# Kernel tuning notes

Hardware: AMD Instinct MI355X
Metric: run time of the kernel (lower is better)

The kernel has to match this reference:

```python
import jax, jax.numpy as jnp
import numpy as np

C = 16      # internal_channel
DG = 8      # deform groups
KK = 9      # 3x3 kernel


def conv2d(x, w, b, pad):
    out = jax.lax.conv_general_dilated(
        x, w, (1, 1), [(pad, pad), (pad, pad)],
        dimension_numbers=('NCHW', 'OIHW', 'NCHW'))
    return out + b[None, :, None, None]


def feature_extraction(img, w1, b1, w2, b2, w3, b3):
    f1 = jax.nn.relu(conv2d(img, w1, b1, 1))   # [B,C,H,W]
    f2 = jax.nn.relu(conv2d(f1, w2, b2, 0))    # [B,C,H-2,W-2]
    f3 = jax.nn.relu(conv2d(f2, w3, b3, 0))    # [B,C,H-4,W-4]
    return [f1, f2, f3]


def deform_conv(x, offset, w, b):
    # x: [B,C,H,W]; offset: [B, DG*KK*2, H, W] (y,x pairs); w: [Cout,C,3,3]
    B, Cin, H, W = x.shape
    Cg = Cin // DG
    off = offset.reshape(B, DG, KK, 2, H, W)
    ky = jnp.repeat(jnp.arange(3) - 1, 3)  # kernel y offsets (pad=1)
    kx = jnp.tile(jnp.arange(3) - 1, 3)
    base_y = jnp.arange(H).reshape(1, 1, 1, H, 1)
    base_x = jnp.arange(W).reshape(1, 1, 1, 1, W)
    sy = base_y + ky.reshape(1, 1, KK, 1, 1) + off[:, :, :, 0]  # [B,DG,KK,H,W]
    sx = base_x + kx.reshape(1, 1, KK, 1, 1) + off[:, :, :, 1]
    y0 = jnp.floor(sy)
    x0 = jnp.floor(sx)
    wy = (sy - y0)[:, :, None]  # [B,DG,1,KK,H,W]
    wx = (sx - x0)[:, :, None]
    y0i = y0.astype(jnp.int32)
    x0i = x0.astype(jnp.int32)
    xg = x.reshape(B, DG, Cg, H * W)

    def gather(yy, xx):
        valid = (yy >= 0) & (yy < H) & (xx >= 0) & (xx < W)  # zero pad outside
        idx = (jnp.clip(yy, 0, H - 1) * W + jnp.clip(xx, 0, W - 1))
        idx_b = jnp.broadcast_to(idx.reshape(B, DG, 1, KK, H * W), (B, DG, Cg, KK, H * W))
        src = jnp.broadcast_to(xg[:, :, :, None, :], (B, DG, Cg, KK, H * W))
        g = jnp.take_along_axis(src, idx_b, axis=-1).reshape(B, DG, Cg, KK, H, W)
        return g * valid[:, :, None].astype(x.dtype)

    v00 = gather(y0i, x0i)
    v01 = gather(y0i, x0i + 1)
    v10 = gather(y0i + 1, x0i)
    v11 = gather(y0i + 1, x0i + 1)
    s = (v00 * (1 - wy) * (1 - wx) + v01 * (1 - wy) * wx
         + v10 * wy * (1 - wx) + v11 * wy * wx)
    s = s.reshape(B, Cin, KK, H, W)
    out = jnp.einsum('bckhw,ock->bohw', s, w.reshape(w.shape[0], Cin, KK))
    return out + b[None, :, None, None]


def setup_inputs() -> dict:
    key = jax.random.key(0)
    ks = jax.random.split(key, 24)
    B, H, W = 4, 192, 192
    sc = 0.05
    d = {
        'ref_image': jax.random.normal(ks[0], (B, C, H, W), jnp.float32),
        'unreg_image': jax.random.normal(ks[1], (B, C, H, W), jnp.float32),
        'fe_w1': jax.random.normal(ks[2], (C, C, 3, 3), jnp.float32) * sc,
        'fe_b1': jnp.zeros((C,), jnp.float32),
        'fe_w2': jax.random.normal(ks[3], (C, C, 3, 3), jnp.float32) * sc,
        'fe_b2': jnp.zeros((C,), jnp.float32),
        'fe_w3': jax.random.normal(ks[4], (C, C, 3, 3), jnp.float32) * sc,
        'fe_b3': jnp.zeros((C,), jnp.float32),
        'off_w0': jax.random.normal(ks[5], (C, 2 * C, 3, 3), jnp.float32) * sc,
        'off_b0': jnp.zeros((C,), jnp.float32),
        'off_w1': jax.random.normal(ks[6], (C, 2 * C, 3, 3), jnp.float32) * sc,
        'off_b1': jnp.zeros((C,), jnp.float32),
        'off_w2': jax.random.normal(ks[7], (C, 2 * C, 3, 3), jnp.float32) * sc,
        'off_b2': jnp.zeros((C,), jnp.float32),
        'dcn_off_w': jax.random.normal(ks[8], (2 * DG * KK, C, 3, 3), jnp.float32) * sc,
        'dcn_off_b': jnp.zeros((2 * DG * KK,), jnp.float32),
        'dcn_w': jax.random.normal(ks[9], (C, C, 3, 3), jnp.float32) * sc,
        'dcn_b': jnp.zeros((C,), jnp.float32),
    }
    return d


def reference(ref_image, unreg_image, fe_w1, fe_b1, fe_w2, fe_b2, fe_w3, fe_b3,
              off_w0, off_b0, off_w1, off_b1, off_w2, off_b2,
              dcn_off_w, dcn_off_b, dcn_w, dcn_b):
    ref_f = feature_extraction(ref_image, fe_w1, fe_b1, fe_w2, fe_b2, fe_w3, fe_b3)
    unr_f = feature_extraction(unreg_image, fe_w1, fe_b1, fe_w2, fe_b2, fe_w3, fe_b3)
    off_ws = [(off_w0, off_b0), (off_w1, off_b1), (off_w2, off_b2)]
    aligned = [None, None, None]
    for i in range(2, -1, -1):  # coarse-to-fine as in the source loop
        cat = jnp.concatenate([ref_f[i], unr_f[i]], axis=1)        # [B,2C,h,w]
        off_feat = jax.nn.relu(conv2d(cat, off_ws[i][0], off_ws[i][1], 1))
        offsets = conv2d(off_feat, dcn_off_w, dcn_off_b, 1)        # [B,2*DG*KK,h,w]
        aligned[i] = deform_conv(unr_f[i], offsets, dcn_w, dcn_b)
    return tuple(aligned)
```

## Files before the change

### kernel.cpp

```cpp
#include <hip/hip_runtime.h>

typedef unsigned int uint;
typedef unsigned short ushort;
typedef __attribute__((ext_vector_type(8))) short bf16x8;
typedef __attribute__((ext_vector_type(4))) float f32x4;

__device__ inline ushort f2bf(float f) {
    uint u = __float_as_uint(f);
    u += 0x7fff + ((u >> 16) & 1);
    return (ushort)(u >> 16);
}
__device__ inline float bflo(uint w) { return __uint_as_float(w << 16); }
__device__ inline float bfhi(uint w) { return __uint_as_float(w & 0xffff0000u); }

__global__ void packall_k(
    const float* __restrict__ fe_w1, const float* __restrict__ fe_w2,
    const float* __restrict__ fe_w3, const float* __restrict__ off_w0,
    const float* __restrict__ off_w1, const float* __restrict__ off_w2,
    const float* __restrict__ dcn_off_w, const float* __restrict__ dcn_w,
    ushort* __restrict__ pf1, ushort* __restrict__ pf2, ushort* __restrict__ pf3,
    ushort* __restrict__ po0, ushort* __restrict__ po1, ushort* __restrict__ po2,
    ushort* __restrict__ pow_, ushort* __restrict__ pd) {
    const int y = blockIdx.y;
    int i = blockIdx.x * 256 + threadIdx.x;
    const float* w; ushort* pk; int CIN, NT, KS;
    switch (y) {
        case 0: w = fe_w1;  pk = pf1;  CIN = 16; NT = 1; KS = 5; break;
        case 1: w = fe_w2;  pk = pf2;  CIN = 16; NT = 1; KS = 5; break;
        case 2: w = fe_w3;  pk = pf3;  CIN = 16; NT = 1; KS = 5; break;
        case 3: w = off_w0; pk = po0;  CIN = 32; NT = 1; KS = 9; break;
        case 4: w = off_w1; pk = po1;  CIN = 32; NT = 1; KS = 9; break;
        case 5: w = off_w2; pk = po2;  CIN = 32; NT = 1; KS = 9; break;
        case 6: w = dcn_off_w; pk = pow_; CIN = 16; NT = 9; KS = 5; break;
        default: w = dcn_w; pk = pd;   CIN = 16; NT = 1; KS = 5; break;
    }
    if (i >= KS * NT * 512) return;
    int e = i & 7, lane = (i >> 3) & 63, rest = i >> 9;
    int nt = rest % NT, ks = rest / NT;
    int k = ks * 32 + (lane >> 4) * 8 + e;
    int n = nt * 16 + (lane & 15);
    int t, ci;
    if (CIN == 16) { t = k >> 4; ci = k & 15; } else { t = k >> 5; ci = k & 31; }
    float v = (t < 9) ? w[(n * CIN + ci) * 9 + t] : 0.f;
    pk[i] = f2bf(v);
}

template <bool PLANAR>
__launch_bounds__(256)
__global__ void fe_mfma_k(const float* __restrict__ pA, const float* __restrict__ pB,
                          const ushort* __restrict__ catin,
                          const ushort* __restrict__ pack, const float* __restrict__ bias,
                          ushort* __restrict__ catout,
                          int H, int W, int OH, int OW, int pad) {
    __shared__ ushort patch[324 * 16];
    const int tid = threadIdx.x;
    const int tx0 = blockIdx.x * 16, ty0 = blockIdx.y * 16;
    const int b = blockIdx.z & 3, img = blockIdx.z >> 2;
    const int bx = tx0 - pad, by = ty0 - pad;
    const int HW = H * W;

    if (PLANAR) {
        const float* inb = (img ? pB : pA) + (size_t)(b * 16) * HW;
        for (int pos = tid; pos < 324; pos += 256) {
            int r = pos / 18, c = pos - r * 18;
            int gy = by + r, gx = bx + c;
            bool ok = (unsigned)gy < (unsigned)H && (unsigned)gx < (unsigned)W;
            int base = gy * W + gx;
            uint o16[8];
#pragma unroll
            for (int ii = 0; ii < 8; ++ii) {
                float lo = ok ? inb[(2 * ii) * HW + base] : 0.f;
                float hi = ok ? inb[(2 * ii + 1) * HW + base] : 0.f;
                o16[ii] = (uint)f2bf(lo) | ((uint)f2bf(hi) << 16);
            }
            *(uint4*)(patch + pos * 16) = *(uint4*)&o16[0];
            *(uint4*)(patch + pos * 16 + 8) = *(uint4*)&o16[4];
        }
    } else {
        for (int c = tid; c < 648; c += 256) {
            int pos = c >> 1, h = c & 1;
            int r = pos / 18, col = pos - r * 18;
            int gy = by + r, gx = bx + col;
            uint4 v = make_uint4(0, 0, 0, 0);
            if ((unsigned)gy < (unsigned)H && (unsigned)gx < (unsigned)W)
                v = *(const uint4*)(catin + ((size_t)(b * H + gy) * W + gx) * 32 + img * 16 + h * 8);
            *(uint4*)(patch + pos * 16 + h * 8) = v;
        }
    }
    __syncthreads();

    const int lane = tid & 63, wv = tid >> 6;
    const int g = lane >> 4, ci0 = (g & 1) * 8, rowx = lane & 15;
    f32x4 acc[4];
    float bv = bias[rowx];
#pragma unroll
    for (int m = 0; m < 4; ++m) acc[m] = f32x4{bv, bv, bv, bv};

#pragma unroll
    for (int ks = 0; ks < 5; ++ks) {
        int t = 2 * ks + (g >> 1);
        int dy = t < 9 ? t / 3 : 0;
        int dx = t < 9 ? t - (t / 3) * 3 : 0;
        bf16x8 a[4];
#pragma unroll
        for (int m = 0; m < 4; ++m) {
            int r = wv * 4 + m + dy, cc = rowx + dx;
            a[m] = *(const bf16x8*)(patch + (r * 18 + cc) * 16 + ci0);
        }
        bf16x8 bfrag = *(const bf16x8*)((const uint4*)pack + ks * 64 + lane);
#pragma unroll
        for (int m = 0; m < 4; ++m)
            acc[m] = __builtin_amdgcn_mfma_f32_16x16x32_bf16(a[m], bfrag, acc[m], 0, 0, 0);
    }

    const int oxb = g * 4;
#pragma unroll
    for (int m = 0; m < 4; ++m) {
        int gy = ty0 + wv * 4 + m;
        if (gy >= OH) continue;
#pragma unroll
        for (int j = 0; j < 4; ++j) {
            int gx = tx0 + oxb + j;
            if (gx < OW)
                catout[((size_t)(b * OH + gy) * OW + gx) * 32 + img * 16 + rowx] =
                    f2bf(fmaxf(acc[m][j], 0.f));
        }
    }
}

__launch_bounds__(256)
__global__ void off_mfma_k(const ushort* __restrict__ c0, const ushort* __restrict__ c1,
                           const ushort* __restrict__ c2,
                           const ushort* __restrict__ pk0, const ushort* __restrict__ pk1,
                           const ushort* __restrict__ pk2,
                           const float* __restrict__ b0, const float* __restrict__ b1,
                           const float* __restrict__ b2,
                           ushort* __restrict__ f0, ushort* __restrict__ f1,
                           ushort* __restrict__ f2) {
    const int z = blockIdx.z, s = z >> 2, b = z & 3;
    const int H = 192 - 2 * s, W = H;
    const ushort* cat  = s == 0 ? c0 : (s == 1 ? c1 : c2);
    const ushort* pack = s == 0 ? pk0 : (s == 1 ? pk1 : pk2);
    const float* bias  = s == 0 ? b0 : (s == 1 ? b1 : b2);
    ushort* out        = s == 0 ? f0 : (s == 1 ? f1 : f2);

    __shared__ ushort patch[324 * 32];
    const int tid = threadIdx.x;
    const int tx0 = blockIdx.x * 16, ty0 = blockIdx.y * 16;
    const int bx = tx0 - 1, by = ty0 - 1;

    for (int c = tid; c < 1296; c += 256) {
        int pos = c >> 2, h = c & 3;
        int r = pos / 18, col = pos - r * 18;
        int gy = by + r, gx = bx + col;
        uint4 v = make_uint4(0, 0, 0, 0);
        if ((unsigned)gy < (unsigned)H && (unsigned)gx < (unsigned)W)
            v = *(const uint4*)(cat + ((size_t)(b * H + gy) * W + gx) * 32 + h * 8);
        *(uint4*)(patch + pos * 32 + h * 8) = v;
    }
    __syncthreads();

    const int lane = tid & 63, wv = tid >> 6;
    const int g = lane >> 4, ci0 = g * 8, rowx = lane & 15;
    f32x4 acc[4];
    float bv = bias[rowx];
#pragma unroll
    for (int m = 0; m < 4; ++m) acc[m] = f32x4{bv, bv, bv, bv};

#pragma unroll
    for (int ks = 0; ks < 9; ++ks) {
        int dy = ks / 3, dx = ks - (ks / 3) * 3;
        bf16x8 a[4];
#pragma unroll
        for (int m = 0; m < 4; ++m) {
            int r = wv * 4 + m + dy, cc = rowx + dx;
            a[m] = *(const bf16x8*)(patch + (r * 18 + cc) * 32 + ci0);
        }
        bf16x8 bfrag = *(const bf16x8*)((const uint4*)pack + ks * 64 + lane);
#pragma unroll
        for (int m = 0; m < 4; ++m)
            acc[m] = __builtin_amdgcn_mfma_f32_16x16x32_bf16(a[m], bfrag, acc[m], 0, 0, 0);
    }

    const int oxb = g * 4;
#pragma unroll
    for (int m = 0; m < 4; ++m) {
        int gy = ty0 + wv * 4 + m;
        if (gy >= H) continue;
#pragma unroll
        for (int j = 0; j < 4; ++j) {
            int gx = tx0 + oxb + j;
            if (gx < W)
                out[((size_t)(b * H + gy) * W + gx) * 16 + rowx] = f2bf(fmaxf(acc[m][j], 0.f));
        }
    }
}

__launch_bounds__(256)
__global__ void offconv_mfma_k(const ushort* __restrict__ fb0, const ushort* __restrict__ fb1,
                               const ushort* __restrict__ fb2,
                               const ushort* __restrict__ owPack, const float* __restrict__ ob,
                               ushort* __restrict__ of0, ushort* __restrict__ of1,
                               ushort* __restrict__ of2, int zbase) {
    const int z = blockIdx.z + zbase;
    const int s = z >> 2, b = z & 3;
    const int H = 192 - 2 * s, W = H;
    const ushort* fb = s == 0 ? fb0 : (s == 1 ? fb1 : fb2);
    ushort* ofs = s == 0 ? of0 : (s == 1 ? of1 : of2);

    __shared__ ushort smem[10240];
    ushort* patch = smem;
    const int tid = threadIdx.x;
    const int tx0 = blockIdx.x * 16, ty0 = blockIdx.y * 16;

    for (int c = tid; c < 648; c += 256) {
        int pos = c >> 1, h = c & 1;
        int r = pos / 18, col = pos - r * 18;
        int gy = ty0 - 1 + r, gx = tx0 - 1 + col;
        uint4 v = make_uint4(0, 0, 0, 0);
        if (gy >= 0 && gy < H && gx >= 0 && gx < W)
            v = *(const uint4*)(fb + ((size_t)(b * H + gy) * W + gx) * 16 + h * 8);
        *(uint4*)(patch + pos * 16 + h * 8) = v;
    }
    __syncthreads();

    const int lane = tid & 63, wv = tid >> 6;
    const int g = lane >> 4, ci0 = (g & 1) * 8, rowx = lane & 15;

    f32x4 acc[4][9];
#pragma unroll
    for (int n = 0; n < 9; ++n) {
        float bv = ob[n * 16 + rowx];
#pragma unroll
        for (int m = 0; m < 4; ++m) acc[m][n] = f32x4{bv, bv, bv, bv};
    }

#pragma unroll
    for (int ks = 0; ks < 5; ++ks) {
        int t = 2 * ks + (g >> 1);
        int dy = t < 9 ? t / 3 : 0;
        int dx = t < 9 ? t - (t / 3) * 3 : 0;
        bf16x8 a[4];
#pragma unroll
        for (int m = 0; m < 4; ++m) {
            int r = wv * 4 + m + dy, cc = rowx + dx;
            a[m] = *(const bf16x8*)(patch + (r * 18 + cc) * 16 + ci0);
        }
        const uint4* bp = (const uint4*)owPack + (size_t)(ks * 9) * 64 + lane;
#pragma unroll
        for (int n = 0; n < 9; ++n) {
            bf16x8 bfrag = *(const bf16x8*)(bp + (size_t)n * 64);
#pragma unroll
            for (int m = 0; m < 4; ++m)
                acc[m][n] = __builtin_amdgcn_mfma_f32_16x16x32_bf16(a[m], bfrag, acc[m][n], 0, 0, 0);
        }
    }
    __syncthreads();

    ushort* ot = smem + wv * 2560;
    const size_t rowbytes_base = (size_t)b * H * W;
#pragma unroll
    for (int m = 0; m < 4; ++m) {
#pragma unroll
        for (int n = 0; n < 9; ++n) {
            int ch = n * 16 + rowx;
            int dg = ch / 18;
            int rem = ch - dg * 18;
            int col = (rem >> 1) * 16 + dg * 2 + (rem & 1);
#pragma unroll
            for (int j = 0; j < 4; ++j)
                ot[(g * 4 + j) * 160 + col] = f2bf(acc[m][n][j]);
        }
        int py = ty0 + wv * 4 + m;
        if (py < H) {
            const uint4* src4 = (const uint4*)ot;
            uint4* dst4 = (uint4*)(ofs + (rowbytes_base + (size_t)py * W + tx0) * 160);
            for (int i = lane; i < 320; i += 64)
                if (tx0 + i / 20 < W) dst4[i] = src4[i];
        }
    }
}

__launch_bounds__(256)
__global__ void sample_mfma_k(const ushort* __restrict__ c0, const ushort* __restrict__ c1,
                              const ushort* __restrict__ c2,
                              const ushort* __restrict__ of0, const ushort* __restrict__ of1,
                              const ushort* __restrict__ of2,
                              const ushort* __restrict__ pd, const float* __restrict__ db,
                              float* __restrict__ o0, float* __restrict__ o1,
                              float* __restrict__ o2, int zbase) {
    const int z = blockIdx.z + zbase;
    const int s = z >> 2, b = z & 3;
    const int H = 192 - 2 * s, W = H;
    const ushort* cat = s == 0 ? c0 : (s == 1 ? c1 : c2);
    const ushort* ofs = s == 0 ? of0 : (s == 1 ? of1 : of2);
    float* out = s == 0 ? o0 : (s == 1 ? o1 : o2);
    const int HW = H * W;
    const size_t pixb = (size_t)b * HW;

    __shared__ float2 xt[8][22 * 22];
    const int tid = threadIdx.x;
    const int tx0 = blockIdx.x * 16, ty0 = blockIdx.y * 16;
    const int bx = tx0 - 3, by = ty0 - 3;

    for (int pos = tid; pos < 484; pos += 256) {
        int r = pos / 22, c = pos - r * 22;
        int gy2 = by + r, gx2 = bx + c;
        uint4 va = make_uint4(0, 0, 0, 0), vb = va;
        if ((unsigned)gy2 < (unsigned)H && (unsigned)gx2 < (unsigned)W) {
            const ushort* src = cat + (pixb + gy2 * W + gx2) * 32 + 16;
            va = *(const uint4*)src;
            vb = *(const uint4*)(src + 8);
        }
        uint u[8] = {va.x, va.y, va.z, va.w, vb.x, vb.y, vb.z, vb.w};
#pragma unroll
        for (int cp = 0; cp < 8; ++cp)
            xt[cp][pos] = make_float2(bflo(u[cp]), bfhi(u[cp]));
    }
    __syncthreads();

    const int lane = tid & 63, wv = tid >> 6;
    const int g = lane >> 4, rowx = lane & 15, half = g & 1;
    const int px = tx0 + rowx;
    const int pxc = px < W ? px : W - 1;

    f32x4 acc[4];
    float bv = db[rowx];
#pragma unroll
    for (int m = 0; m < 4; ++m) acc[m] = f32x4{bv, bv, bv, bv};

#pragma unroll 1
    for (int ks = 0; ks < 5; ++ks) {
        const int t = 2 * ks + (g >> 1);
        const bool tv = (t < 9);
        const int t3 = t / 3;
        const int ky = (tv ? t3 : 0) - 1, kx = (tv ? t - t3 * 3 : 0) - 1;

        uint4 ovm[4];
#pragma unroll
        for (int m = 0; m < 4; ++m) {
            int py = ty0 + wv * 4 + m;
            int pyc = py < H ? py : H - 1;
            ovm[m] = tv ? *(const uint4*)(ofs + (pixb + pyc * W + pxc) * 160 + t * 16 + half * 8)
                        : make_uint4(0, 0, 0, 0);
        }
        bf16x8 bfrag = *(const bf16x8*)((const uint4*)pd + ks * 64 + lane);

#pragma unroll
        for (int m = 0; m < 4; ++m) {
            const int py = ty0 + wv * 4 + m;
            uint ovv[4] = {ovm[m].x, ovm[m].y, ovm[m].z, ovm[m].w};
            uint a2[4];
            if (tv) {
#pragma unroll
                for (int d = 0; d < 4; ++d) {
                    const int dgA = half * 4 + d;
                    uint u = ovv[d];
                    float sy = (float)(py + ky) + bflo(u);
                    float sx = (float)(px + kx) + bfhi(u);
                    float fy = floorf(sy), fx = floorf(sx);
                    int y0 = (int)fy, x0 = (int)fx;
                    float wy = sy - fy, wx = sx - fx;
                    float wy1 = 1.f - wy, wx1 = 1.f - wx;
                    float w00 = wy1 * wx1, w01 = wy1 * wx, w10 = wy * wx1, w11 = wy * wx;
                    int ly = y0 - by, lx = x0 - bx;
                    float2 v00, v01, v10, v11;
                    if ((unsigned)ly <= 20u && (unsigned)lx <= 20u) {
                        const float2* tt = &xt[dgA][ly * 22 + lx];
                        v00 = tt[0]; v01 = tt[1]; v10 = tt[22]; v11 = tt[23];
                    } else {
                        v00 = v01 = v10 = v11 = make_float2(0.f, 0.f);
                        bool y0v = (unsigned)y0 < (unsigned)H;
                        bool y1v = (unsigned)(y0 + 1) < (unsigned)H;
                        bool x0v = (unsigned)x0 < (unsigned)W;
                        bool x1v = (unsigned)(x0 + 1) < (unsigned)W;
                        const ushort* cg = cat + ((size_t)pixb + (size_t)y0 * W + x0) * 32 + 16 + 2 * dgA;
                        if (y0v && x0v) { uint uu = *(const uint*)cg;                 v00 = make_float2(bflo(uu), bfhi(uu)); }
                        if (y0v && x1v) { uint uu = *(const uint*)(cg + 32);          v01 = make_float2(bflo(uu), bfhi(uu)); }
                        if (y1v && x0v) { uint uu = *(const uint*)(cg + 32 * W);      v10 = make_float2(bflo(uu), bfhi(uu)); }
                        if (y1v && x1v) { uint uu = *(const uint*)(cg + 32 * W + 32); v11 = make_float2(bflo(uu), bfhi(uu)); }
                    }
                    float s0 = w00 * v00.x + w01 * v01.x + w10 * v10.x + w11 * v11.x;
                    float s1 = w00 * v00.y + w01 * v01.y + w10 * v10.y + w11 * v11.y;
                    a2[d] = (uint)f2bf(s0) | ((uint)f2bf(s1) << 16);
                }
            } else {
                a2[0] = a2[1] = a2[2] = a2[3] = 0u;
            }
            uint4 av = make_uint4(a2[0], a2[1], a2[2], a2[3]);
            bf16x8 af = *(bf16x8*)&av;
            acc[m] = __builtin_amdgcn_mfma_f32_16x16x32_bf16(af, bfrag, acc[m], 0, 0, 0);
        }
    }

#pragma unroll
    for (int m = 0; m < 4; ++m) {
        int py = ty0 + wv * 4 + m;
        if (py >= H) continue;
        float* op = out + (size_t)(b * 16 + rowx) * HW + (size_t)py * W;
#pragma unroll
        for (int j = 0; j < 4; ++j) {
            int gx2 = tx0 + g * 4 + j;
            if (gx2 < W) op[gx2] = acc[m][j];
        }
    }
}

extern "C" void kernel_launch(void* const* d_in, const int* in_sizes, int n_in,
                              void* d_out, int out_size, void* d_ws, size_t ws_size,
                              hipStream_t stream) {
    const float* ref_image = (const float*)d_in[0];
    const float* unreg_image = (const float*)d_in[1];
    const float* fe_w1 = (const float*)d_in[2];
    const float* fe_b1 = (const float*)d_in[3];
    const float* fe_w2 = (const float*)d_in[4];
    const float* fe_b2 = (const float*)d_in[5];
    const float* fe_w3 = (const float*)d_in[6];
    const float* fe_b3 = (const float*)d_in[7];
    const float* off_w0 = (const float*)d_in[8];
    const float* off_b0 = (const float*)d_in[9];
    const float* off_w1 = (const float*)d_in[10];
    const float* off_b1 = (const float*)d_in[11];
    const float* off_w2 = (const float*)d_in[12];
    const float* off_b2 = (const float*)d_in[13];
    const float* dcn_off_w = (const float*)d_in[14];
    const float* dcn_off_b = (const float*)d_in[15];
    const float* dcn_w = (const float*)d_in[16];
    const float* dcn_b = (const float*)d_in[17];

    const size_t pix[3] = {4ul * 192 * 192, 4ul * 190 * 190, 4ul * 188 * 188};
    const size_t szf[3] = {pix[0] * 16, pix[1] * 16, pix[2] * 16};

    size_t o = 0;
    auto take = [&](size_t bytes) {
        void* r = (char*)d_ws + o;
        o += (bytes + 255) & ~(size_t)255;
        return r;
    };
    ushort* cat[3]; ushort* fb[3];
    ushort* pf[3]; ushort* po[3]; ushort* owPack; ushort* pd;
    for (int s = 0; s < 3; ++s) cat[s] = (ushort*)take(pix[s] * 32 * 2);
    for (int s = 0; s < 3; ++s) fb[s] = (ushort*)take(pix[s] * 16 * 2);
    for (int s = 0; s < 3; ++s) pf[s] = (ushort*)take(2560 * 2);
    for (int s = 0; s < 3; ++s) po[s] = (ushort*)take(4608 * 2);
    owPack = (ushort*)take(23040 * 2);
    pd = (ushort*)take(2560 * 2);

    ushort* offsBuf[3];
    size_t need3 = o;
    for (int s = 0; s < 3; ++s) need3 += (pix[s] * 320 + 255) & ~(size_t)255;
    bool batched = (ws_size >= need3);
    if (batched) {
        for (int s = 0; s < 3; ++s) offsBuf[s] = (ushort*)take(pix[s] * 320);
    } else {
        ushort* one = (ushort*)take(pix[0] * 320);
        offsBuf[0] = offsBuf[1] = offsBuf[2] = one;
    }

    float* out0 = (float*)d_out;
    float* out1 = out0 + szf[0];
    float* out2 = out1 + szf[1];

    dim3 blk(256);

    packall_k<<<dim3(90, 8), blk, 0, stream>>>(
        fe_w1, fe_w2, fe_w3, off_w0, off_w1, off_w2, dcn_off_w, dcn_w,
        pf[0], pf[1], pf[2], po[0], po[1], po[2], owPack, pd);

    fe_mfma_k<true><<<dim3(12, 12, 8), blk, 0, stream>>>(
        ref_image, unreg_image, nullptr, pf[0], fe_b1, cat[0], 192, 192, 192, 192, 1);
    fe_mfma_k<false><<<dim3(12, 12, 8), blk, 0, stream>>>(
        nullptr, nullptr, cat[0], pf[1], fe_b2, cat[1], 192, 192, 190, 190, 0);
    fe_mfma_k<false><<<dim3(12, 12, 8), blk, 0, stream>>>(
        nullptr, nullptr, cat[1], pf[2], fe_b3, cat[2], 190, 190, 188, 188, 0);

    off_mfma_k<<<dim3(12, 12, 12), blk, 0, stream>>>(
        cat[0], cat[1], cat[2], po[0], po[1], po[2],
        off_b0, off_b1, off_b2, fb[0], fb[1], fb[2]);

    if (batched) {
        offconv_mfma_k<<<dim3(12, 12, 12), blk, 0, stream>>>(
            fb[0], fb[1], fb[2], owPack, dcn_off_b,
            offsBuf[0], offsBuf[1], offsBuf[2], 0);
        sample_mfma_k<<<dim3(12, 12, 12), blk, 0, stream>>>(
            cat[0], cat[1], cat[2], offsBuf[0], offsBuf[1], offsBuf[2],
            pd, dcn_b, out0, out1, out2, 0);
    } else {
        for (int s = 0; s < 3; ++s) {
            offconv_mfma_k<<<dim3(12, 12, 4), blk, 0, stream>>>(
                fb[0], fb[1], fb[2], owPack, dcn_off_b,
                offsBuf[0], offsBuf[1], offsBuf[2], 4 * s);
            sample_mfma_k<<<dim3(12, 12, 4), blk, 0, stream>>>(
                cat[0], cat[1], cat[2], offsBuf[0], offsBuf[1], offsBuf[2],
                pd, dcn_b, out0, out1, out2, 4 * s);
        }
    }
}
```

Measured before the change: 185.1 us.

## Fuse offset convolution and deformable sampling into one kernel via shared memory

Merges the offset-producing conv kernel and the deformable sampling/MFMA kernel into a single kernel. Per-row offsets now stay in LDS instead of going to a global workspace (160 bf16 channels per pixel) and being read back. This removes a large global write and read plus one launch. In exchange, shared memory per block grows to about 52KB, which can cut occupancy, and the sampling work is now serialised after the conv inside each block.

Result: slower. 196.8 us (+6.3%).

```diff
diff --git a/kernel.cpp b/kernel.cpp
--- a/kernel.cpp
+++ b/kernel.cpp
@@ -197,19 +197,27 @@
 }
 
 __launch_bounds__(256)
-__global__ void offconv_mfma_k(const ushort* __restrict__ fb0, const ushort* __restrict__ fb1,
-                               const ushort* __restrict__ fb2,
-                               const ushort* __restrict__ owPack, const float* __restrict__ ob,
-                               ushort* __restrict__ of0, ushort* __restrict__ of1,
-                               ushort* __restrict__ of2, int zbase) {
-    const int z = blockIdx.z + zbase;
+__global__ void dcn_fused_k(const ushort* __restrict__ c0, const ushort* __restrict__ c1,
+                            const ushort* __restrict__ c2,
+                            const ushort* __restrict__ fb0, const ushort* __restrict__ fb1,
+                            const ushort* __restrict__ fb2,
+                            const ushort* __restrict__ owPack, const float* __restrict__ ob,
+                            const ushort* __restrict__ pd, const float* __restrict__ db,
+                            float* __restrict__ o0, float* __restrict__ o1,
+                            float* __restrict__ o2) {
+    const int z = blockIdx.z;
     const int s = z >> 2, b = z & 3;
     const int H = 192 - 2 * s, W = H;
-    const ushort* fb = s == 0 ? fb0 : (s == 1 ? fb1 : fb2);
-    ushort* ofs = s == 0 ? of0 : (s == 1 ? of1 : of2);
-
-    __shared__ ushort smem[10240];
+    const ushort* cat = s == 0 ? c0 : (s == 1 ? c1 : c2);
+    const ushort* fb  = s == 0 ? fb0 : (s == 1 ? fb1 : fb2);
+    float* out        = s == 0 ? o0 : (s == 1 ? o1 : o2);
+    const int HW = H * W;
+    const size_t pixb = (size_t)b * HW;
+
+    __shared__ ushort smem[26240];
     ushort* patch = smem;
+    float2* xt = (float2*)(smem + 10752);
+
     const int tid = threadIdx.x;
     const int tx0 = blockIdx.x * 16, ty0 = blockIdx.y * 16;
 
@@ -218,14 +226,32 @@
         int r = pos / 18, col = pos - r * 18;
         int gy = ty0 - 1 + r, gx = tx0 - 1 + col;
         uint4 v = make_uint4(0, 0, 0, 0);
-        if (gy >= 0 && gy < H && gx >= 0 && gx < W)
+        if ((unsigned)gy < (unsigned)H && (unsigned)gx < (unsigned)W)
             v = *(const uint4*)(fb + ((size_t)(b * H + gy) * W + gx) * 16 + h * 8);
         *(uint4*)(patch + pos * 16 + h * 8) = v;
     }
+    {
+        const int bx3 = tx0 - 3, by3 = ty0 - 3;
+        for (int pos = tid; pos < 484; pos += 256) {
+            int r = pos / 22, c = pos - r * 22;
+            int gy2 = by3 + r, gx2 = bx3 + c;
+            uint4 va = make_uint4(0, 0, 0, 0), vb = va;
+            if ((unsigned)gy2 < (unsigned)H && (unsigned)gx2 < (unsigned)W) {
+                const ushort* src = cat + (pixb + gy2 * W + gx2) * 32 + 16;
+                va = *(const uint4*)src;
+                vb = *(const uint4*)(src + 8);
+            }
+            uint u[8] = {va.x, va.y, va.z, va.w, vb.x, vb.y, vb.z, vb.w};
+#pragma unroll
+            for (int cp = 0; cp < 8; ++cp)
+                xt[cp * 484 + pos] = make_float2(bflo(u[cp]), bfhi(u[cp]));
+        }
+    }
     __syncthreads();
 
     const int lane = tid & 63, wv = tid >> 6;
-    const int g = lane >> 4, ci0 = (g & 1) * 8, rowx = lane & 15;
+    const int g = lane >> 4, rowx = lane & 15, half = g & 1;
+    const int ci0 = half * 8;
 
     f32x4 acc[4][9];
 #pragma unroll
@@ -257,8 +283,10 @@
     }
     __syncthreads();
 
-    ushort* ot = smem + wv * 2560;
-    const size_t rowbytes_base = (size_t)b * H * W;
+    ushort* ot = smem + wv * 2688;
+    const int px = tx0 + rowx;
+    const float bv2 = db[rowx];
+
 #pragma unroll
     for (int m = 0; m < 4; ++m) {
 #pragma unroll
@@ -269,89 +297,23 @@
             int col = (rem >> 1) * 16 + dg * 2 + (rem & 1);
 #pragma unroll
             for (int j = 0; j < 4; ++j)
-                ot[(g * 4 + j) * 160 + col] = f2bf(acc[m][n][j]);
-        }
-        int py = ty0 + wv * 4 + m;
-        if (py < H) {
-            const uint4* src4 = (const uint4*)ot;
-            uint4* dst4 = (uint4*)(ofs + (rowbytes_base + (size_t)py * W + tx0) * 160);
-            for (int i = lane; i < 320; i += 64)
-                if (tx0 + i / 20 < W) dst4[i] = src4[i];
-        }
-    }
-}
-
-__launch_bounds__(256)
-__global__ void sample_mfma_k(const ushort* __restrict__ c0, const ushort* __restrict__ c1,
-                              const ushort* __restrict__ c2,
-                              const ushort* __restrict__ of0, const ushort* __restrict__ of1,
-                              const ushort* __restrict__ of2,
-                              const ushort* __restrict__ pd, const float* __restrict__ db,
-                              float* __restrict__ o0, float* __restrict__ o1,
-                              float* __restrict__ o2, int zbase) {
-    const int z = blockIdx.z + zbase;
-    const int s = z >> 2, b = z & 3;
-    const int H = 192 - 2 * s, W = H;
-    const ushort* cat = s == 0 ? c0 : (s == 1 ? c1 : c2);
-    const ushort* ofs = s == 0 ? of0 : (s == 1 ? of1 : of2);
-    float* out = s == 0 ? o0 : (s == 1 ? o1 : o2);
-    const int HW = H * W;
-    const size_t pixb = (size_t)b * HW;
-
-    __shared__ float2 xt[8][22 * 22];
-    const int tid = threadIdx.x;
-    const int tx0 = blockIdx.x * 16, ty0 = blockIdx.y * 16;
-    const int bx = tx0 - 3, by = ty0 - 3;
-
-    for (int pos = tid; pos < 484; pos += 256) {
-        int r = pos / 22, c = pos - r * 22;
-        int gy2 = by + r, gx2 = bx + c;
-        uint4 va = make_uint4(0, 0, 0, 0), vb = va;
-        if ((unsigned)gy2 < (unsigned)H && (unsigned)gx2 < (unsigned)W) {
-            const ushort* src = cat + (pixb + gy2 * W + gx2) * 32 + 16;
-            va = *(const uint4*)src;
-            vb = *(const uint4*)(src + 8);
-        }
-        uint u[8] = {va.x, va.y, va.z, va.w, vb.x, vb.y, vb.z, vb.w};
-#pragma unroll
-        for (int cp = 0; cp < 8; ++cp)
-            xt[cp][pos] = make_float2(bflo(u[cp]), bfhi(u[cp]));
-    }
-    __syncthreads();
-
-    const int lane = tid & 63, wv = tid >> 6;
-    const int g = lane >> 4, rowx = lane & 15, half = g & 1;
-    const int px = tx0 + rowx;
-    const int pxc = px < W ? px : W - 1;
-
-    f32x4 acc[4];
-    float bv = db[rowx];
-#pragma unroll
-    for (int m = 0; m < 4; ++m) acc[m] = f32x4{bv, bv, bv, bv};
+                ot[(g * 4 + j) * 168 + col] = f2bf(acc[m][n][j]);
+        }
+
+        const int py = ty0 + wv * 4 + m;
+        f32x4 acc2 = f32x4{bv2, bv2, bv2, bv2};
 
 #pragma unroll 1
-    for (int ks = 0; ks < 5; ++ks) {
-        const int t = 2 * ks + (g >> 1);
-        const bool tv = (t < 9);
-        const int t3 = t / 3;
-        const int ky = (tv ? t3 : 0) - 1, kx = (tv ? t - t3 * 3 : 0) - 1;
-
-        uint4 ovm[4];
-#pragma unroll
-        for (int m = 0; m < 4; ++m) {
-            int py = ty0 + wv * 4 + m;
-            int pyc = py < H ? py : H - 1;
-            ovm[m] = tv ? *(const uint4*)(ofs + (pixb + pyc * W + pxc) * 160 + t * 16 + half * 8)
-                        : make_uint4(0, 0, 0, 0);
-        }
-        bf16x8 bfrag = *(const bf16x8*)((const uint4*)pd + ks * 64 + lane);
-
-#pragma unroll
-        for (int m = 0; m < 4; ++m) {
-            const int py = ty0 + wv * 4 + m;
-            uint ovv[4] = {ovm[m].x, ovm[m].y, ovm[m].z, ovm[m].w};
+        for (int ks = 0; ks < 5; ++ks) {
+            const int t = 2 * ks + (g >> 1);
+            const bool tv = (t < 9);
+            const int t3 = t / 3;
+            const int ky = (tv ? t3 : 0) - 1, kx = (tv ? t - t3 * 3 : 0) - 1;
+
             uint a2[4];
             if (tv) {
+                uint4 ov = *(const uint4*)(ot + rowx * 168 + t * 16 + half * 8);
+                uint ovv[4] = {ov.x, ov.y, ov.z, ov.w};
 #pragma unroll
                 for (int d = 0; d < 4; ++d) {
                     const int dgA = half * 4 + d;
@@ -363,10 +325,10 @@
                     float wy = sy - fy, wx = sx - fx;
                     float wy1 = 1.f - wy, wx1 = 1.f - wx;
                     float w00 = wy1 * wx1, w01 = wy1 * wx, w10 = wy * wx1, w11 = wy * wx;
-                    int ly = y0 - by, lx = x0 - bx;
+                    int ly = y0 - (ty0 - 3), lx = x0 - (tx0 - 3);
                     float2 v00, v01, v10, v11;
                     if ((unsigned)ly <= 20u && (unsigned)lx <= 20u) {
-                        const float2* tt = &xt[dgA][ly * 22 + lx];
+                        const float2* tt = &xt[dgA * 484 + ly * 22 + lx];
                         v00 = tt[0]; v01 = tt[1]; v10 = tt[22]; v11 = tt[23];
                     } else {
                         v00 = v01 = v10 = v11 = make_float2(0.f, 0.f);
@@ -389,19 +351,17 @@
             }
             uint4 av = make_uint4(a2[0], a2[1], a2[2], a2[3]);
             bf16x8 af = *(bf16x8*)&av;
-            acc[m] = __builtin_amdgcn_mfma_f32_16x16x32_bf16(af, bfrag, acc[m], 0, 0, 0);
-        }
-    }
-
-#pragma unroll
-    for (int m = 0; m < 4; ++m) {
-        int py = ty0 + wv * 4 + m;
-        if (py >= H) continue;
-        float* op = out + (size_t)(b * 16 + rowx) * HW + (size_t)py * W;
-#pragma unroll
-        for (int j = 0; j < 4; ++j) {
-            int gx2 = tx0 + g * 4 + j;
-            if (gx2 < W) op[gx2] = acc[m][j];
+            bf16x8 dfrag = *(const bf16x8*)((const uint4*)pd + ks * 64 + lane);
+            acc2 = __builtin_amdgcn_mfma_f32_16x16x32_bf16(af, dfrag, acc2, 0, 0, 0);
+        }
+
+        if (py < H) {
+            float* op = out + (size_t)(b * 16 + rowx) * HW + (size_t)py * W;
+#pragma unroll
+            for (int j = 0; j < 4; ++j) {
+                int gx2 = tx0 + g * 4 + j;
+                if (gx2 < W) op[gx2] = acc2[j];
+            }
         }
     }
 }
@@ -446,17 +406,6 @@
     owPack = (ushort*)take(23040 * 2);
     pd = (ushort*)take(2560 * 2);
 
-    ushort* offsBuf[3];
-    size_t need3 = o;
-    for (int s = 0; s < 3; ++s) need3 += (pix[s] * 320 + 255) & ~(size_t)255;
-    bool batched = (ws_size >= need3);
-    if (batched) {
-        for (int s = 0; s < 3; ++s) offsBuf[s] = (ushort*)take(pix[s] * 320);
-    } else {
-        ushort* one = (ushort*)take(pix[0] * 320);
-        offsBuf[0] = offsBuf[1] = offsBuf[2] = one;
-    }
-
     float* out0 = (float*)d_out;
     float* out1 = out0 + szf[0];
     float* out2 = out1 + szf[1];
@@ -478,21 +427,7 @@
         cat[0], cat[1], cat[2], po[0], po[1], po[2],
         off_b0, off_b1, off_b2, fb[0], fb[1], fb[2]);
 
-    if (batched) {
-        offconv_mfma_k<<<dim3(12, 12, 12), blk, 0, stream>>>(
-            fb[0], fb[1], fb[2], owPack, dcn_off_b,
-            offsBuf[0], offsBuf[1], offsBuf[2], 0);
-        sample_mfma_k<<<dim3(12, 12, 12), blk, 0, stream>>>(
-            cat[0], cat[1], cat[2], offsBuf[0], offsBuf[1], offsBuf[2],
-            pd, dcn_b, out0, out1, out2, 0);
-    } else {
-        for (int s = 0; s < 3; ++s) {
-            offconv_mfma_k<<<dim3(12, 12, 4), blk, 0, stream>>>(
-                fb[0], fb[1], fb[2], owPack, dcn_off_b,
-                offsBuf[0], offsBuf[1], offsBuf[2], 4 * s);
-            sample_mfma_k<<<dim3(12, 12, 4), blk, 0, stream>>>(
-                cat[0], cat[1], cat[2], offsBuf[0], offsBuf[1], offsBuf[2],
-                pd, dcn_b, out0, out1, out2, 4 * s);
-        }
-    }
-}
+    dcn_fused_k<<<dim3(12, 12, 12), blk, 0, stream>>>(
+        cat[0], cat[1], cat[2], fb[0], fb[1], fb[2],
+        owPack, dcn_off_b, pd, dcn_b, out0, out1, out2);
+}
```
